# Optimization experiments

Measured on AMD Instinct MI355X. Metric: run time of the kernel, lower is better.

## Reference

```python
import jax, jax.numpy as jnp
import numpy as np

NP, NC, F, H = 50000, 10000, 128, 256
E_ANNO, E_LINK, E_PPI, NPAIR = 250000, 100000, 500000, 4096


def _sage(x_src, x_dst, src, dst, Wl, b, Wr):
    # PyG SAGEConv(aggr='mean'): lin_l(mean of gathered neighbor feats) + lin_r(x_dst)
    n_dst = x_dst.shape[0]
    agg = jax.ops.segment_sum(x_src[src], dst, num_segments=n_dst)
    cnt = jax.ops.segment_sum(jnp.ones((src.shape[0], 1), x_src.dtype), dst, num_segments=n_dst)
    mean = agg / jnp.maximum(cnt, 1.0)  # isolated dst nodes get 0
    return mean @ Wl.T + b + x_dst @ Wr.T


def setup_inputs():
    key = jax.random.key(0)
    ks = iter(jax.random.split(key, 64))
    s = 0.05
    inp = {}
    inp['x_protein'] = jax.random.normal(next(ks), (NP, F), jnp.float32)
    inp['x_class'] = jax.random.normal(next(ks), (NC, F), jnp.float32)
    for layer, din, dout in [('a', F, H), ('b', H, F)]:
        for rel in ['annop', 'annon', 'link', 'ppi']:
            inp[f'{layer}_{rel}_Wl'] = jax.random.normal(next(ks), (dout, din), jnp.float32) * s
            inp[f'{layer}_{rel}_b'] = jax.random.normal(next(ks), (dout,), jnp.float32) * s
            inp[f'{layer}_{rel}_Wr'] = jax.random.normal(next(ks), (dout, din), jnp.float32) * s
    inp['lin_W'] = jax.random.normal(next(ks), (1, 2 * F), jnp.float32) * s
    inp['lin_b'] = jnp.zeros((1,), jnp.float32)
    inp['annop_src'] = jax.random.randint(next(ks), (E_ANNO,), 0, NP)
    inp['annop_dst'] = jax.random.randint(next(ks), (E_ANNO,), 0, NC)
    inp['annon_src'] = jax.random.randint(next(ks), (E_ANNO,), 0, NP)
    inp['annon_dst'] = jax.random.randint(next(ks), (E_ANNO,), 0, NC)
    inp['link_src'] = jax.random.randint(next(ks), (E_LINK,), 0, NC)
    inp['link_dst'] = jax.random.randint(next(ks), (E_LINK,), 0, NC)
    inp['ppi_src'] = jax.random.randint(next(ks), (E_PPI,), 0, NP)
    inp['ppi_dst'] = jax.random.randint(next(ks), (E_PPI,), 0, NP)
    inp['mask'] = jax.random.randint(next(ks), (NPAIR, 2), 0, NP)
    return inp


def reference(x_protein, x_class,
              a_annop_Wl, a_annop_b, a_annop_Wr,
              a_annon_Wl, a_annon_b, a_annon_Wr,
              a_link_Wl, a_link_b, a_link_Wr,
              a_ppi_Wl, a_ppi_b, a_ppi_Wr,
              b_annop_Wl, b_annop_b, b_annop_Wr,
              b_annon_Wl, b_annon_b, b_annon_Wr,
              b_link_Wl, b_link_b, b_link_Wr,
              b_ppi_Wl, b_ppi_b, b_ppi_Wr,
              lin_W, lin_b,
              annop_src, annop_dst, annon_src, annon_dst,
              link_src, link_dst, ppi_src, ppi_dst, mask):
    # Layer 1 (HeteroConv aggregates per dst node type with sum)
    hc = (_sage(x_protein, x_class, annop_src, annop_dst, a_annop_Wl, a_annop_b, a_annop_Wr)
          + _sage(x_protein, x_class, annon_src, annon_dst, a_annon_Wl, a_annon_b, a_annon_Wr)
          + _sage(x_class, x_class, link_src, link_dst, a_link_Wl, a_link_b, a_link_Wr))
    hp = _sage(x_protein, x_protein, ppi_src, ppi_dst, a_ppi_Wl, a_ppi_b, a_ppi_Wr)
    hc = jax.nn.relu(hc)
    hp = jax.nn.relu(hp)
    # Layer 2
    hp2 = _sage(hp, hp, ppi_src, ppi_dst, b_ppi_Wl, b_ppi_b, b_ppi_Wr)
    # (class outputs of layer 2 are computed in the original but unused for the head)
    hc2 = (_sage(hp, hc, annop_src, annop_dst, b_annop_Wl, b_annop_b, b_annop_Wr)
           + _sage(hp, hc, annon_src, annon_dst, b_annon_Wl, b_annon_b, b_annon_Wr)
           + _sage(hc, hc, link_src, link_dst, b_link_Wl, b_link_b, b_link_Wr))
    del hc2
    # Pair readout: mask.T -> rows of protein indices; original detaches p1, p2
    p1 = jax.lax.stop_gradient(hp2[mask[:, 0]])
    p2 = jax.lax.stop_gradient(hp2[mask[:, 1]])
    h = jnp.concatenate((p1, p2), axis=1)  # [NPAIR, 2F]
    return jax.nn.sigmoid(h @ lin_W.T + lin_b)
```

## Files before the change

kernel.cpp:

```cpp
#include <hip/hip_runtime.h>
#include <math.h>

#define NPROT 50000
#define NPROT_PAD 50048
#define EPPI 500000
#define NPAIR 4096

typedef __attribute__((ext_vector_type(8))) __bf16 bf16x8;
typedef __attribute__((ext_vector_type(4))) __bf16 bf16x4;
typedef __attribute__((ext_vector_type(4))) float floatx4;

__global__ void k_hist(const int* __restrict__ dst, int* __restrict__ cnt) {
    int e = blockIdx.x * 256 + threadIdx.x;
    if (e < EPPI) atomicAdd(&cnt[dst[e]], 1);
}

__global__ void k_scan1(const int* __restrict__ cnt, int* __restrict__ rowptr,
                        int* __restrict__ blocksum) {
    __shared__ int sd[1024];
    int t = threadIdx.x;
    int i = blockIdx.x * 1024 + t;
    int v = (i < NPROT) ? cnt[i] : 0;
    sd[t] = v;
    __syncthreads();
    int x = v;
    for (int off = 1; off < 1024; off <<= 1) {
        int add = (t >= off) ? sd[t - off] : 0;
        __syncthreads();
        x += add;
        sd[t] = x;
        __syncthreads();
    }
    if (i < NPROT) rowptr[i] = x - v;
    if (t == 1023) blocksum[blockIdx.x] = x;
}

__global__ void k_scan3(const int* __restrict__ cnt, int* __restrict__ rowptr,
                        int* __restrict__ cursor, float* __restrict__ inv,
                        const int* __restrict__ blocksum, int nb) {
    __shared__ int spref;
    int t = threadIdx.x;
    if (t < 64) {
        int v = (t < blockIdx.x && t < nb) ? blocksum[t] : 0;
#pragma unroll
        for (int m = 1; m < 64; m <<= 1) v += __shfl_xor(v, m, 64);
        if (t == 0) spref = v;
    }
    __syncthreads();
    int i = blockIdx.x * 1024 + t;
    if (i < NPROT) {
        int r = rowptr[i] + spref;
        rowptr[i] = r;
        cursor[i] = r;
        int c = cnt[i];
        inv[i] = 1.0f / (float)(c > 1 ? c : 1);
        if (i == NPROT - 1) rowptr[NPROT] = r + c;
    }
}

__global__ void k_fill(const int* __restrict__ src, const int* __restrict__ dst,
                       int* __restrict__ cursor, int* __restrict__ ssrc) {
    int e = blockIdx.x * 256 + threadIdx.x;
    if (e < EPPI) {
        int d = dst[e];
        int p = atomicAdd(&cursor[d], 1);
        ssrc[p] = src[e];
    }
}

__global__ void k_prep(const float* __restrict__ x,
                       const float* __restrict__ Wl, const float* __restrict__ Wr,
                       const float* __restrict__ linW, const float* __restrict__ linb,
                       const float* __restrict__ bWl, const float* __restrict__ bWr,
                       const float* __restrict__ bb,
                       __bf16* __restrict__ Xb, __bf16* __restrict__ Bw,
                       float* __restrict__ P, float* __restrict__ biasC,
                       int* __restrict__ cnt) {
    int b = blockIdx.x, t = threadIdx.x;
    if (b < 6250) {
        int i = b * 256 + t;
        int row = i >> 5, k4 = (i & 31) << 2;
        float4 v = *(const float4*)(x + (size_t)row * 128 + k4);
        bf16x4 o; o[0] = (__bf16)v.x; o[1] = (__bf16)v.y; o[2] = (__bf16)v.z; o[3] = (__bf16)v.w;
        *(bf16x4*)(Xb + (size_t)row * 128 + k4) = o;
    } else if (b < 6506) {
        int idx = (b - 6250) * 256 + t;
        int h = idx >> 8, k = idx & 255;
        float v = (k < 128) ? Wl[h * 128 + k] : Wr[h * 128 + (k - 128)];
        Bw[idx] = (__bf16)v;
    } else if (b == 6506) {
        int h = t;
        float v1 = 0, v2 = 0, u1 = 0, u2 = 0;
        for (int f = 0; f < 128; f++) {
            float w1 = linW[f], w2 = linW[128 + f];
            float wl = bWl[f * 256 + h], wr = bWr[f * 256 + h];
            v1 += w1 * wl; v2 += w2 * wl; u1 += w1 * wr; u2 += w2 * wr;
        }
        P[h * 4 + 0] = v1; P[h * 4 + 1] = v2; P[h * 4 + 2] = u1; P[h * 4 + 3] = u2;
        if (h == 0) {
            float c = linb[0];
            for (int f = 0; f < 128; f++) c += (linW[f] + linW[128 + f]) * bb[f];
            *biasC = c;
        }
    } else {
        int i = (b - 6507) * 256 + t;
        if (i < NPROT) cnt[i] = 0;
    }
}

__global__ void k_agg(const __bf16* __restrict__ Xb, const int* __restrict__ rowptr,
                      const int* __restrict__ ssrc, const float* __restrict__ inv,
                      __bf16* __restrict__ Am) {
    int wave = threadIdx.x >> 6, lane = threadIdx.x & 63;
    int q = lane >> 4, sl = lane & 15;
    int node = blockIdx.x * 16 + wave * 4 + q;
    if (node >= NPROT) return;
    int b0 = rowptr[node], b1 = rowptr[node + 1];
    float a[8];
#pragma unroll
    for (int e = 0; e < 8; e++) a[e] = 0.f;
    const __bf16* base = Xb + (size_t)sl * 8;
    int j = b0;
    for (; j + 4 <= b1; j += 4) {
        int s0 = ssrc[j], s1 = ssrc[j + 1], s2 = ssrc[j + 2], s3 = ssrc[j + 3];
        bf16x8 v0 = *(const bf16x8*)(base + (size_t)s0 * 128);
        bf16x8 v1 = *(const bf16x8*)(base + (size_t)s1 * 128);
        bf16x8 v2 = *(const bf16x8*)(base + (size_t)s2 * 128);
        bf16x8 v3 = *(const bf16x8*)(base + (size_t)s3 * 128);
#pragma unroll
        for (int e = 0; e < 8; e++)
            a[e] += ((float)v0[e] + (float)v1[e]) + ((float)v2[e] + (float)v3[e]);
    }
    for (; j < b1; j++) {
        int s = ssrc[j];
        bf16x8 v = *(const bf16x8*)(base + (size_t)s * 128);
#pragma unroll
        for (int e = 0; e < 8; e++) a[e] += (float)v[e];
    }
    float iv = inv[node];
    bf16x8 o;
#pragma unroll
    for (int e = 0; e < 8; e++) o[e] = (__bf16)(a[e] * iv);
    *(bf16x8*)(Am + (size_t)node * 128 + sl * 8) = o;
}

__global__ __launch_bounds__(256) void k_gemm(const __bf16* __restrict__ Am,
                                              const __bf16* __restrict__ Xb,
                                              const __bf16* __restrict__ Bw,
                                              const float* __restrict__ ab,
                                              const float* __restrict__ P,
                                              float* __restrict__ y) {
    __shared__ __bf16 Bs[2048 * 8];
    int tid = threadIdx.x;
    int wave = tid >> 6, lane = tid & 63;
    int r = lane & 15, quad = lane >> 4;
    int row0 = blockIdx.x * 128 + wave * 32;

    bf16x8 afrag[2][8];
#pragma unroll
    for (int g = 0; g < 2; g++) {
        const __bf16* mp = Am + (size_t)(row0 + g * 16 + r) * 128 + quad * 8;
        const __bf16* op = Xb + (size_t)(row0 + g * 16 + r) * 128 + quad * 8;
#pragma unroll
        for (int kk = 0; kk < 4; kk++) {
            afrag[g][kk]     = *(const bf16x8*)(mp + kk * 32);
            afrag[g][4 + kk] = *(const bf16x8*)(op + kk * 32);
        }
    }

    float part[2][4][4] = {{{0.f}}};

    for (int chunk = 0; chunk < 4; chunk++) {
        if (chunk) __syncthreads();
#pragma unroll
        for (int jj = 0; jj < 8; jj++) {
            int g = jj * 256 + tid;
            int gr = g & 15, gq = (g >> 4) & 3;
            int gkk = (g >> 6) & 7;
            int gt = g >> 9;
            const __bf16* src = Bw + (size_t)(chunk * 64 + gt * 16 + gr) * 256 + gkk * 32 + gq * 8;
            *(bf16x8*)(Bs + (size_t)g * 8) = *(const bf16x8*)src;
        }
        __syncthreads();

        floatx4 acc[2][4];
#pragma unroll
        for (int g = 0; g < 2; g++)
#pragma unroll
            for (int t = 0; t < 4; t++) acc[g][t] = (floatx4){0.f, 0.f, 0.f, 0.f};
#pragma unroll
        for (int kk = 0; kk < 8; kk++) {
#pragma unroll
            for (int t = 0; t < 4; t++) {
                bf16x8 bf = *(const bf16x8*)(Bs + (size_t)((t * 8 + kk) * 64 + lane) * 8);
                acc[0][t] = __builtin_amdgcn_mfma_f32_16x16x32_bf16(afrag[0][kk], bf, acc[0][t], 0, 0, 0);
                acc[1][t] = __builtin_amdgcn_mfma_f32_16x16x32_bf16(afrag[1][kk], bf, acc[1][t], 0, 0, 0);
            }
        }

#pragma unroll
        for (int t = 0; t < 4; t++) {
            int col = chunk * 64 + t * 16 + r;
            float bias = ab[col];
            float4 pv = *(const float4*)(P + col * 4);
#pragma unroll
            for (int g = 0; g < 2; g++)
#pragma unroll
                for (int rr = 0; rr < 4; rr++) {
                    float h = acc[g][t][rr] + bias;
                    h = h > 0.f ? h : 0.f;
                    part[g][rr][0] += h * pv.x; part[g][rr][1] += h * pv.y;
                    part[g][rr][2] += h * pv.z; part[g][rr][3] += h * pv.w;
                }
        }
    }

#pragma unroll
    for (int m = 1; m < 16; m <<= 1)
#pragma unroll
        for (int g = 0; g < 2; g++)
#pragma unroll
            for (int rr = 0; rr < 4; rr++)
#pragma unroll
                for (int j = 0; j < 4; j++)
                    part[g][rr][j] += __shfl_xor(part[g][rr][j], m, 64);
    if (r == 0) {
#pragma unroll
        for (int g = 0; g < 2; g++)
#pragma unroll
            for (int rr = 0; rr < 4; rr++) {
                int row = row0 + g * 16 + quad * 4 + rr;
                float4 o;
                o.x = part[g][rr][0]; o.y = part[g][rr][1];
                o.z = part[g][rr][2]; o.w = part[g][rr][3];
                *(float4*)(y + (size_t)row * 4) = o;
            }
    }
}

__global__ void k_head(const int* __restrict__ mask, const int* __restrict__ rowptr,
                       const int* __restrict__ ssrc, const float* __restrict__ inv,
                       const float* __restrict__ y, const float* __restrict__ biasC,
                       float* __restrict__ out) {
    int tid = blockIdx.x * 256 + threadIdx.x;
    int p = tid >> 1, side = tid & 1;
    float res = 0.f;
    if (p < NPAIR) {
        int node = mask[p * 2 + side];
        int b0 = rowptr[node], b1 = rowptr[node + 1];
        float s = 0.f;
        for (int j = b0; j < b1; j++) s += y[(size_t)ssrc[j] * 4 + side];
        res = s * inv[node] + y[(size_t)node * 4 + 2 + side];
    }
    float other = __shfl_xor(res, 1, 64);
    if (p < NPAIR && side == 0) {
        float z = res + other + *biasC;
        out[p] = 1.f / (1.f + expf(-z));
    }
}

extern "C" void kernel_launch(void* const* d_in, const int* in_sizes, int n_in,
                              void* d_out, int out_size, void* d_ws, size_t ws_size,
                              hipStream_t stream) {
    const float* x_protein = (const float*)d_in[0];
    const float* a_ppi_Wl  = (const float*)d_in[11];
    const float* a_ppi_b   = (const float*)d_in[12];
    const float* a_ppi_Wr  = (const float*)d_in[13];
    const float* b_ppi_Wl  = (const float*)d_in[23];
    const float* b_ppi_b   = (const float*)d_in[24];
    const float* b_ppi_Wr  = (const float*)d_in[25];
    const float* lin_W     = (const float*)d_in[26];
    const float* lin_b     = (const float*)d_in[27];
    const int* ppi_src     = (const int*)d_in[34];
    const int* ppi_dst     = (const int*)d_in[35];
    const int* mask        = (const int*)d_in[36];
    float* out = (float*)d_out;

    char* ws = (char*)d_ws;
    size_t o = 0;
    auto alloc = [&](size_t n) -> char* {
        char* r = ws + o;
        o = (o + n + 511) & ~(size_t)511;
        return r;
    };
    int*    cnt      = (int*)alloc((size_t)NPROT * 4);
    int*    rowptr   = (int*)alloc((size_t)(NPROT + 1) * 4);
    int*    cursor   = (int*)alloc((size_t)NPROT * 4);
    int*    blocksum = (int*)alloc(64 * 4);
    float*  inv      = (float*)alloc((size_t)NPROT * 4);
    int*    ssrc     = (int*)alloc((size_t)EPPI * 4);
    __bf16* Xb       = (__bf16*)alloc((size_t)NPROT_PAD * 128 * 2);
    __bf16* Am       = (__bf16*)alloc((size_t)NPROT_PAD * 128 * 2);
    __bf16* Bw       = (__bf16*)alloc(256 * 256 * 2);
    float*  P        = (float*)alloc(256 * 4 * 4);
    float*  biasC    = (float*)alloc(4);
    float*  y        = (float*)alloc((size_t)NPROT_PAD * 4 * 4);
    (void)ws_size;

    int nb = (NPROT + 1023) / 1024;

    k_prep<<<6703, 256, 0, stream>>>(x_protein, a_ppi_Wl, a_ppi_Wr, lin_W, lin_b,
                                     b_ppi_Wl, b_ppi_Wr, b_ppi_b,
                                     Xb, Bw, P, biasC, cnt);
    k_hist<<<(EPPI + 255) / 256, 256, 0, stream>>>(ppi_dst, cnt);
    k_scan1<<<nb, 1024, 0, stream>>>(cnt, rowptr, blocksum);
    k_scan3<<<nb, 1024, 0, stream>>>(cnt, rowptr, cursor, inv, blocksum, nb);
    k_fill<<<(EPPI + 255) / 256, 256, 0, stream>>>(ppi_src, ppi_dst, cursor, ssrc);
    k_agg<<<(NPROT + 15) / 16, 256, 0, stream>>>(Xb, rowptr, ssrc, inv, Am);
    k_gemm<<<(NPROT_PAD + 127) / 128, 256, 0, stream>>>(Am, Xb, Bw, a_ppi_b, P, y);
    k_head<<<(2 * NPAIR + 255) / 256, 256, 0, stream>>>(mask, rowptr, ssrc, inv, y, biasC, out);
}
```

Measured before the change: 260.9 us.

## Fuse prep, histogram, scan and CSR fill into one cooperative kernel

Replaces five separate launches (prep, hist, two scan passes, fill) with a single cooperative kernel of 256 blocks that uses grid-wide syncs between phases. The aim is to remove launch overhead and inter-kernel gaps. The cost is that the whole grid only has 256 blocks, so the bf16 conversion and the atomic phases run with grid-stride loops at lower parallelism. The P precompute is also reparallelised across blocks using wave reductions.

New measurement: 408.9 us. +56.7%, slower.

```diff
diff --git a/kernel.cpp b/kernel.cpp
--- a/kernel.cpp
+++ b/kernel.cpp
@@ -1,5 +1,8 @@
 #include <hip/hip_runtime.h>
+#include <hip/hip_cooperative_groups.h>
 #include <math.h>
+
+namespace cg = cooperative_groups;
 
 #define NPROT 50000
 #define NPROT_PAD 50048
@@ -10,101 +13,103 @@
 typedef __attribute__((ext_vector_type(4))) __bf16 bf16x4;
 typedef __attribute__((ext_vector_type(4))) float floatx4;
 
-__global__ void k_hist(const int* __restrict__ dst, int* __restrict__ cnt) {
-    int e = blockIdx.x * 256 + threadIdx.x;
-    if (e < EPPI) atomicAdd(&cnt[dst[e]], 1);
-}
-
-__global__ void k_scan1(const int* __restrict__ cnt, int* __restrict__ rowptr,
-                        int* __restrict__ blocksum) {
-    __shared__ int sd[1024];
-    int t = threadIdx.x;
-    int i = blockIdx.x * 1024 + t;
-    int v = (i < NPROT) ? cnt[i] : 0;
-    sd[t] = v;
-    __syncthreads();
-    int x = v;
-    for (int off = 1; off < 1024; off <<= 1) {
-        int add = (t >= off) ? sd[t - off] : 0;
-        __syncthreads();
-        x += add;
-        sd[t] = x;
-        __syncthreads();
-    }
-    if (i < NPROT) rowptr[i] = x - v;
-    if (t == 1023) blocksum[blockIdx.x] = x;
-}
-
-__global__ void k_scan3(const int* __restrict__ cnt, int* __restrict__ rowptr,
+__global__ void k_build(const float* __restrict__ x,
+                        const float* __restrict__ Wl, const float* __restrict__ Wr,
+                        const float* __restrict__ linW, const float* __restrict__ linb,
+                        const float* __restrict__ bWl, const float* __restrict__ bWr,
+                        const float* __restrict__ bb,
+                        const int* __restrict__ src, const int* __restrict__ dst,
+                        __bf16* __restrict__ Xb, __bf16* __restrict__ Bw,
+                        float* __restrict__ P, float* __restrict__ biasC,
+                        int* __restrict__ cnt, int* __restrict__ rowptr,
                         int* __restrict__ cursor, float* __restrict__ inv,
-                        const int* __restrict__ blocksum, int nb) {
-    __shared__ int spref;
-    int t = threadIdx.x;
-    if (t < 64) {
-        int v = (t < blockIdx.x && t < nb) ? blocksum[t] : 0;
-#pragma unroll
-        for (int m = 1; m < 64; m <<= 1) v += __shfl_xor(v, m, 64);
-        if (t == 0) spref = v;
-    }
-    __syncthreads();
-    int i = blockIdx.x * 1024 + t;
-    if (i < NPROT) {
-        int r = rowptr[i] + spref;
-        rowptr[i] = r;
-        cursor[i] = r;
-        int c = cnt[i];
-        inv[i] = 1.0f / (float)(c > 1 ? c : 1);
-        if (i == NPROT - 1) rowptr[NPROT] = r + c;
-    }
-}
-
-__global__ void k_fill(const int* __restrict__ src, const int* __restrict__ dst,
-                       int* __restrict__ cursor, int* __restrict__ ssrc) {
-    int e = blockIdx.x * 256 + threadIdx.x;
-    if (e < EPPI) {
-        int d = dst[e];
-        int p = atomicAdd(&cursor[d], 1);
-        ssrc[p] = src[e];
-    }
-}
-
-__global__ void k_prep(const float* __restrict__ x,
-                       const float* __restrict__ Wl, const float* __restrict__ Wr,
-                       const float* __restrict__ linW, const float* __restrict__ linb,
-                       const float* __restrict__ bWl, const float* __restrict__ bWr,
-                       const float* __restrict__ bb,
-                       __bf16* __restrict__ Xb, __bf16* __restrict__ Bw,
-                       float* __restrict__ P, float* __restrict__ biasC,
-                       int* __restrict__ cnt) {
+                        int* __restrict__ blocksum, int* __restrict__ ssrc) {
+    cg::grid_group grid = cg::this_grid();
+    __shared__ int sd[256];
+    __shared__ float sP[12];
     int b = blockIdx.x, t = threadIdx.x;
-    if (b < 6250) {
-        int i = b * 256 + t;
+    int gid = b * 256 + t;
+    int lane = t & 63, wave = t >> 6;
+
+    if (gid < NPROT) cnt[gid] = 0;
+    for (int i = gid; i < NPROT * 32; i += 65536) {
         int row = i >> 5, k4 = (i & 31) << 2;
         float4 v = *(const float4*)(x + (size_t)row * 128 + k4);
         bf16x4 o; o[0] = (__bf16)v.x; o[1] = (__bf16)v.y; o[2] = (__bf16)v.z; o[3] = (__bf16)v.w;
         *(bf16x4*)(Xb + (size_t)row * 128 + k4) = o;
-    } else if (b < 6506) {
-        int idx = (b - 6250) * 256 + t;
-        int h = idx >> 8, k = idx & 255;
+    }
+    {
+        int h = gid >> 8, k = gid & 255;
         float v = (k < 128) ? Wl[h * 128 + k] : Wr[h * 128 + (k - 128)];
-        Bw[idx] = (__bf16)v;
-    } else if (b == 6506) {
-        int h = t;
-        float v1 = 0, v2 = 0, u1 = 0, u2 = 0;
-        for (int f = 0; f < 128; f++) {
-            float w1 = linW[f], w2 = linW[128 + f];
-            float wl = bWl[f * 256 + h], wr = bWr[f * 256 + h];
-            v1 += w1 * wl; v2 += w2 * wl; u1 += w1 * wr; u2 += w2 * wr;
-        }
-        P[h * 4 + 0] = v1; P[h * 4 + 1] = v2; P[h * 4 + 2] = u1; P[h * 4 + 3] = u2;
-        if (h == 0) {
-            float c = linb[0];
-            for (int f = 0; f < 128; f++) c += (linW[f] + linW[128 + f]) * bb[f];
-            *biasC = c;
-        }
-    } else {
-        int i = (b - 6507) * 256 + t;
-        if (i < NPROT) cnt[i] = 0;
+        Bw[gid] = (__bf16)v;
+    }
+    {
+        float v1 = 0, v2 = 0, u1 = 0, u2 = 0, c = 0;
+        if (t < 128) {
+            float w1 = linW[t], w2 = linW[128 + t];
+            float wl = bWl[t * 256 + b], wr = bWr[t * 256 + b];
+            v1 = w1 * wl; v2 = w2 * wl; u1 = w1 * wr; u2 = w2 * wr;
+            if (b == 0) c = (w1 + w2) * bb[t];
+        }
+#pragma unroll
+        for (int m = 1; m < 64; m <<= 1) {
+            v1 += __shfl_xor(v1, m, 64); v2 += __shfl_xor(v2, m, 64);
+            u1 += __shfl_xor(u1, m, 64); u2 += __shfl_xor(u2, m, 64);
+            c  += __shfl_xor(c, m, 64);
+        }
+        if (lane == 0 && wave < 2) {
+            sP[wave * 6 + 0] = v1; sP[wave * 6 + 1] = v2;
+            sP[wave * 6 + 2] = u1; sP[wave * 6 + 3] = u2;
+            sP[wave * 6 + 4] = c;
+        }
+        __syncthreads();
+        if (t == 0) {
+            P[b * 4 + 0] = sP[0] + sP[6]; P[b * 4 + 1] = sP[1] + sP[7];
+            P[b * 4 + 2] = sP[2] + sP[8]; P[b * 4 + 3] = sP[3] + sP[9];
+            if (b == 0) *biasC = linb[0] + sP[4] + sP[10];
+        }
+    }
+    grid.sync();
+
+    for (int e = gid; e < EPPI; e += 65536) atomicAdd(&cnt[dst[e]], 1);
+    grid.sync();
+
+    int v = (gid < NPROT) ? cnt[gid] : 0;
+    sd[t] = v;
+    __syncthreads();
+    int xv = v;
+    for (int off = 1; off < 256; off <<= 1) {
+        int add = (t >= off) ? sd[t - off] : 0;
+        __syncthreads();
+        xv += add;
+        sd[t] = xv;
+        __syncthreads();
+    }
+    if (t == 255) blocksum[b] = xv;
+    grid.sync();
+    {
+        int pv = (t < b) ? blocksum[t] : 0;
+        __syncthreads();
+        sd[t] = pv;
+        __syncthreads();
+        for (int off = 128; off > 0; off >>= 1) {
+            if (t < off) sd[t] += sd[t + off];
+            __syncthreads();
+        }
+        int r = sd[0] + xv - v;
+        if (gid < NPROT) {
+            rowptr[gid] = r;
+            cursor[gid] = r;
+            inv[gid] = 1.0f / (float)(v > 1 ? v : 1);
+            if (gid == NPROT - 1) rowptr[NPROT] = r + v;
+        }
+    }
+    grid.sync();
+
+    for (int e = gid; e < EPPI; e += 65536) {
+        int d = dst[e];
+        int p = atomicAdd(&cursor[d], 1);
+        ssrc[p] = src[e];
     }
 }
 
@@ -286,7 +291,7 @@
     int*    cnt      = (int*)alloc((size_t)NPROT * 4);
     int*    rowptr   = (int*)alloc((size_t)(NPROT + 1) * 4);
     int*    cursor   = (int*)alloc((size_t)NPROT * 4);
-    int*    blocksum = (int*)alloc(64 * 4);
+    int*    blocksum = (int*)alloc(256 * 4);
     float*  inv      = (float*)alloc((size_t)NPROT * 4);
     int*    ssrc     = (int*)alloc((size_t)EPPI * 4);
     __bf16* Xb       = (__bf16*)alloc((size_t)NPROT_PAD * 128 * 2);
@@ -297,15 +302,16 @@
     float*  y        = (float*)alloc((size_t)NPROT_PAD * 4 * 4);
     (void)ws_size;
 
-    int nb = (NPROT + 1023) / 1024;
-
-    k_prep<<<6703, 256, 0, stream>>>(x_protein, a_ppi_Wl, a_ppi_Wr, lin_W, lin_b,
-                                     b_ppi_Wl, b_ppi_Wr, b_ppi_b,
-                                     Xb, Bw, P, biasC, cnt);
-    k_hist<<<(EPPI + 255) / 256, 256, 0, stream>>>(ppi_dst, cnt);
-    k_scan1<<<nb, 1024, 0, stream>>>(cnt, rowptr, blocksum);
-    k_scan3<<<nb, 1024, 0, stream>>>(cnt, rowptr, cursor, inv, blocksum, nb);
-    k_fill<<<(EPPI + 255) / 256, 256, 0, stream>>>(ppi_src, ppi_dst, cursor, ssrc);
+    void* args[] = {
+        (void*)&x_protein, (void*)&a_ppi_Wl, (void*)&a_ppi_Wr,
+        (void*)&lin_W, (void*)&lin_b, (void*)&b_ppi_Wl, (void*)&b_ppi_Wr, (void*)&b_ppi_b,
+        (void*)&ppi_src, (void*)&ppi_dst,
+        (void*)&Xb, (void*)&Bw, (void*)&P, (void*)&biasC,
+        (void*)&cnt, (void*)&rowptr, (void*)&cursor, (void*)&inv,
+        (void*)&blocksum, (void*)&ssrc,
+    };
+    hipLaunchCooperativeKernel((void*)k_build, dim3(256), dim3(256), args, 0, stream);
+
     k_agg<<<(NPROT + 15) / 16, 256, 0, stream>>>(Xb, rowptr, ssrc, inv, Am);
     k_gemm<<<(NPROT_PAD + 127) / 128, 256, 0, stream>>>(Am, Xb, Bw, a_ppi_b, P, y);
     k_head<<<(2 * NPAIR + 255) / 256, 256, 0, stream>>>(mask, rowptr, ssrc, inv, y, biasC, out);
```

## Replace CSR build with atomic linked-list adjacency per destination node

Applied to the files above, without the earlier changes.

Drops the histogram, two-pass scan and fill kernels that built a CSR structure. In their place, one kernel uses atomicExch on per-node heads to thread each edge into a linked list. Aggregation and the head kernel walk these lists and count degree on the fly. This removes three launches and their passes over the edges, but it turns the gather into a serial pointer chase with dependent loads, so each neighbor fetch can no longer be unrolled or overlapped.

Result: faster. 242.6 us (-7.0%).

```diff
diff --git a/kernel.cpp b/kernel.cpp
--- a/kernel.cpp
+++ b/kernel.cpp
@@ -9,64 +9,6 @@
 typedef __attribute__((ext_vector_type(8))) __bf16 bf16x8;
 typedef __attribute__((ext_vector_type(4))) __bf16 bf16x4;
 typedef __attribute__((ext_vector_type(4))) float floatx4;
-
-__global__ void k_hist(const int* __restrict__ dst, int* __restrict__ cnt) {
-    int e = blockIdx.x * 256 + threadIdx.x;
-    if (e < EPPI) atomicAdd(&cnt[dst[e]], 1);
-}
-
-__global__ void k_scan1(const int* __restrict__ cnt, int* __restrict__ rowptr,
-                        int* __restrict__ blocksum) {
-    __shared__ int sd[1024];
-    int t = threadIdx.x;
-    int i = blockIdx.x * 1024 + t;
-    int v = (i < NPROT) ? cnt[i] : 0;
-    sd[t] = v;
-    __syncthreads();
-    int x = v;
-    for (int off = 1; off < 1024; off <<= 1) {
-        int add = (t >= off) ? sd[t - off] : 0;
-        __syncthreads();
-        x += add;
-        sd[t] = x;
-        __syncthreads();
-    }
-    if (i < NPROT) rowptr[i] = x - v;
-    if (t == 1023) blocksum[blockIdx.x] = x;
-}
-
-__global__ void k_scan3(const int* __restrict__ cnt, int* __restrict__ rowptr,
-                        int* __restrict__ cursor, float* __restrict__ inv,
-                        const int* __restrict__ blocksum, int nb) {
-    __shared__ int spref;
-    int t = threadIdx.x;
-    if (t < 64) {
-        int v = (t < blockIdx.x && t < nb) ? blocksum[t] : 0;
-#pragma unroll
-        for (int m = 1; m < 64; m <<= 1) v += __shfl_xor(v, m, 64);
-        if (t == 0) spref = v;
-    }
-    __syncthreads();
-    int i = blockIdx.x * 1024 + t;
-    if (i < NPROT) {
-        int r = rowptr[i] + spref;
-        rowptr[i] = r;
-        cursor[i] = r;
-        int c = cnt[i];
-        inv[i] = 1.0f / (float)(c > 1 ? c : 1);
-        if (i == NPROT - 1) rowptr[NPROT] = r + c;
-    }
-}
-
-__global__ void k_fill(const int* __restrict__ src, const int* __restrict__ dst,
-                       int* __restrict__ cursor, int* __restrict__ ssrc) {
-    int e = blockIdx.x * 256 + threadIdx.x;
-    if (e < EPPI) {
-        int d = dst[e];
-        int p = atomicAdd(&cursor[d], 1);
-        ssrc[p] = src[e];
-    }
-}
 
 __global__ void k_prep(const float* __restrict__ x,
                        const float* __restrict__ Wl, const float* __restrict__ Wr,
@@ -75,7 +17,7 @@
                        const float* __restrict__ bb,
                        __bf16* __restrict__ Xb, __bf16* __restrict__ Bw,
                        float* __restrict__ P, float* __restrict__ biasC,
-                       int* __restrict__ cnt) {
+                       int* __restrict__ head) {
     int b = blockIdx.x, t = threadIdx.x;
     if (b < 6250) {
         int i = b * 256 + t;
@@ -104,43 +46,47 @@
         }
     } else {
         int i = (b - 6507) * 256 + t;
-        if (i < NPROT) cnt[i] = 0;
-    }
-}
-
-__global__ void k_agg(const __bf16* __restrict__ Xb, const int* __restrict__ rowptr,
-                      const int* __restrict__ ssrc, const float* __restrict__ inv,
+        if (i < NPROT) head[i] = -1;
+    }
+}
+
+__global__ void k_link(const int* __restrict__ src, const int* __restrict__ dst,
+                       int* __restrict__ head, int2* __restrict__ elist) {
+    int e = blockIdx.x * 256 + threadIdx.x;
+    if (e < EPPI) {
+        int d = dst[e];
+        int prev = atomicExch(&head[d], e);
+        elist[e] = make_int2(src[e], prev);
+    }
+}
+
+__global__ void k_agg(const __bf16* __restrict__ Xb, const int* __restrict__ head,
+                      const int2* __restrict__ elist, float* __restrict__ inv,
                       __bf16* __restrict__ Am) {
     int wave = threadIdx.x >> 6, lane = threadIdx.x & 63;
     int q = lane >> 4, sl = lane & 15;
     int node = blockIdx.x * 16 + wave * 4 + q;
     if (node >= NPROT) return;
-    int b0 = rowptr[node], b1 = rowptr[node + 1];
     float a[8];
 #pragma unroll
-    for (int e = 0; e < 8; e++) a[e] = 0.f;
+    for (int e8 = 0; e8 < 8; e8++) a[e8] = 0.f;
     const __bf16* base = Xb + (size_t)sl * 8;
-    int j = b0;
-    for (; j + 4 <= b1; j += 4) {
-        int s0 = ssrc[j], s1 = ssrc[j + 1], s2 = ssrc[j + 2], s3 = ssrc[j + 3];
-        bf16x8 v0 = *(const bf16x8*)(base + (size_t)s0 * 128);
-        bf16x8 v1 = *(const bf16x8*)(base + (size_t)s1 * 128);
-        bf16x8 v2 = *(const bf16x8*)(base + (size_t)s2 * 128);
-        bf16x8 v3 = *(const bf16x8*)(base + (size_t)s3 * 128);
-#pragma unroll
-        for (int e = 0; e < 8; e++)
-            a[e] += ((float)v0[e] + (float)v1[e]) + ((float)v2[e] + (float)v3[e]);
-    }
-    for (; j < b1; j++) {
-        int s = ssrc[j];
-        bf16x8 v = *(const bf16x8*)(base + (size_t)s * 128);
-#pragma unroll
-        for (int e = 0; e < 8; e++) a[e] += (float)v[e];
-    }
-    float iv = inv[node];
+    int e = head[node];
+    int c = 0;
+    while (e >= 0) {
+        int2 el = elist[e];
+        bf16x8 v = *(const bf16x8*)(base + (size_t)el.x * 128);
+#pragma unroll
+        for (int e8 = 0; e8 < 8; e8++) a[e8] += (float)v[e8];
+        c++;
+        e = el.y;
+    }
+    float iv = 1.0f / (float)(c > 1 ? c : 1);
+    if (sl == 0 && q == 0) {  }
+    if (sl == 0) inv[node] = iv;
     bf16x8 o;
 #pragma unroll
-    for (int e = 0; e < 8; e++) o[e] = (__bf16)(a[e] * iv);
+    for (int e8 = 0; e8 < 8; e8++) o[e8] = (__bf16)(a[e8] * iv);
     *(bf16x8*)(Am + (size_t)node * 128 + sl * 8) = o;
 }
 
@@ -238,19 +184,25 @@
     }
 }
 
-__global__ void k_head(const int* __restrict__ mask, const int* __restrict__ rowptr,
-                       const int* __restrict__ ssrc, const float* __restrict__ inv,
-                       const float* __restrict__ y, const float* __restrict__ biasC,
-                       float* __restrict__ out) {
+__global__ void k_head(const int* __restrict__ mask, const int* __restrict__ head,
+                       const int2* __restrict__ elist, const float* __restrict__ y,
+                       const float* __restrict__ biasC, float* __restrict__ out) {
     int tid = blockIdx.x * 256 + threadIdx.x;
     int p = tid >> 1, side = tid & 1;
     float res = 0.f;
     if (p < NPAIR) {
         int node = mask[p * 2 + side];
-        int b0 = rowptr[node], b1 = rowptr[node + 1];
+        int e = head[node];
         float s = 0.f;
-        for (int j = b0; j < b1; j++) s += y[(size_t)ssrc[j] * 4 + side];
-        res = s * inv[node] + y[(size_t)node * 4 + 2 + side];
+        int c = 0;
+        while (e >= 0) {
+            int2 el = elist[e];
+            s += y[(size_t)el.x * 4 + side];
+            c++;
+            e = el.y;
+        }
+        float iv = 1.0f / (float)(c > 1 ? c : 1);
+        res = s * iv + y[(size_t)node * 4 + 2 + side];
     }
     float other = __shfl_xor(res, 1, 64);
     if (p < NPAIR && side == 0) {
@@ -283,30 +235,22 @@
         o = (o + n + 511) & ~(size_t)511;
         return r;
     };
-    int*    cnt      = (int*)alloc((size_t)NPROT * 4);
-    int*    rowptr   = (int*)alloc((size_t)(NPROT + 1) * 4);
-    int*    cursor   = (int*)alloc((size_t)NPROT * 4);
-    int*    blocksum = (int*)alloc(64 * 4);
-    float*  inv      = (float*)alloc((size_t)NPROT * 4);
-    int*    ssrc     = (int*)alloc((size_t)EPPI * 4);
-    __bf16* Xb       = (__bf16*)alloc((size_t)NPROT_PAD * 128 * 2);
-    __bf16* Am       = (__bf16*)alloc((size_t)NPROT_PAD * 128 * 2);
-    __bf16* Bw       = (__bf16*)alloc(256 * 256 * 2);
-    float*  P        = (float*)alloc(256 * 4 * 4);
-    float*  biasC    = (float*)alloc(4);
-    float*  y        = (float*)alloc((size_t)NPROT_PAD * 4 * 4);
+    int*    head   = (int*)alloc((size_t)NPROT * 4);
+    int2*   elist  = (int2*)alloc((size_t)EPPI * 8);
+    float*  inv    = (float*)alloc((size_t)NPROT * 4);
+    __bf16* Xb     = (__bf16*)alloc((size_t)NPROT_PAD * 128 * 2);
+    __bf16* Am     = (__bf16*)alloc((size_t)NPROT_PAD * 128 * 2);
+    __bf16* Bw     = (__bf16*)alloc(256 * 256 * 2);
+    float*  P      = (float*)alloc(256 * 4 * 4);
+    float*  biasC  = (float*)alloc(4);
+    float*  y      = (float*)alloc((size_t)NPROT_PAD * 4 * 4);
     (void)ws_size;
-
-    int nb = (NPROT + 1023) / 1024;
 
     k_prep<<<6703, 256, 0, stream>>>(x_protein, a_ppi_Wl, a_ppi_Wr, lin_W, lin_b,
                                      b_ppi_Wl, b_ppi_Wr, b_ppi_b,
-                                     Xb, Bw, P, biasC, cnt);
-    k_hist<<<(EPPI + 255) / 256, 256, 0, stream>>>(ppi_dst, cnt);
-    k_scan1<<<nb, 1024, 0, stream>>>(cnt, rowptr, blocksum);
-    k_scan3<<<nb, 1024, 0, stream>>>(cnt, rowptr, cursor, inv, blocksum, nb);
-    k_fill<<<(EPPI + 255) / 256, 256, 0, stream>>>(ppi_src, ppi_dst, cursor, ssrc);
-    k_agg<<<(NPROT + 15) / 16, 256, 0, stream>>>(Xb, rowptr, ssrc, inv, Am);
+                                     Xb, Bw, P, biasC, head);
+    k_link<<<(EPPI + 255) / 256, 256, 0, stream>>>(ppi_src, ppi_dst, head, elist);
+    k_agg<<<(NPROT + 15) / 16, 256, 0, stream>>>(Xb, head, elist, inv, Am);
     k_gemm<<<(NPROT_PAD + 127) / 128, 256, 0, stream>>>(Am, Xb, Bw, a_ppi_b, P, y);
-    k_head<<<(2 * NPAIR + 255) / 256, 256, 0, stream>>>(mask, rowptr, ssrc, inv, y, biasC, out);
-}
+    k_head<<<(2 * NPAIR + 255) / 256, 256, 0, stream>>>(mask, head, elist, y, biasC, out);
+}
```
